# Kernel optimization log

Measured on AMD Instinct MI355X. Metric: run time of the kernel, lower is better.

Reference implementation:

```python
import jax, jax.numpy as jnp
import numpy as np

EPS = 1e-5  # BatchNorm2d default eps


def _median_pool3x3(x):
    # x: [B,1,H,W]; 3x3 kernel, stride 1, pad 1 (zero padding, matching F.unfold).
    B, C, H, W = x.shape
    xp = jnp.pad(x, ((0, 0), (0, 0), (1, 1), (1, 1)))
    # Stack the 9 shifted views -> [B,C,H,W,9]; torch.median returns the LOWER
    # median, i.e. sorted index (9-1)//2 = 4 for 9 elements.
    patches = jnp.stack([xp[:, :, i:i + H, j:j + W]
                         for i in range(3) for j in range(3)], axis=-1)
    return jnp.sort(patches, axis=-1)[..., 4]


def _batchnorm_train(x, w, b):
    # BatchNorm2d(1) in training mode: biased variance over (B,H,W) per channel.
    m = jnp.mean(x, axis=(0, 2, 3), keepdims=True)
    v = jnp.mean((x - m) ** 2, axis=(0, 2, 3), keepdims=True)
    return (x - m) * jax.lax.rsqrt(v + EPS) * w.reshape(1, -1, 1, 1) + b.reshape(1, -1, 1, 1)


def _shift_grid_sample(x, xshift, yshift):
    # Faithful to Shift.forward + F.grid_sample(mode='bilinear',
    # padding_mode='zeros', align_corners=False).
    B, C, Nv, Nh = x.shape
    yreg = (jnp.arange(Nv, dtype=x.dtype) - yshift) * 10.0  # [Nv]
    xreg = (jnp.arange(Nh, dtype=x.dtype) - xshift) * 10.0  # [Nh]
    Hv, Wv = Nv * 10.0, Nh * 10.0  # virtual upsampled size used for normalization
    gy = 2.0 * yreg / Hv - 1.0
    gx = 2.0 * xreg / Wv - 1.0
    # unnormalize (align_corners=False): pix = ((g+1)*size - 1)/2
    iy = ((gy + 1.0) * Nv - 1.0) * 0.5  # [Nv]
    ix = ((gx + 1.0) * Nh - 1.0) * 0.5  # [Nh]
    IY, IX = jnp.meshgrid(iy, ix, indexing='ij')  # [Nv,Nh] each

    x0 = jnp.floor(IX); x1 = x0 + 1.0
    y0 = jnp.floor(IY); y1 = y0 + 1.0
    wx1 = IX - x0; wx0 = 1.0 - wx1
    wy1 = IY - y0; wy0 = 1.0 - wy1

    def gather(yc, xc):
        valid = ((yc >= 0) & (yc < Nv) & (xc >= 0) & (xc < Nh)).astype(x.dtype)
        yi = jnp.clip(yc, 0, Nv - 1).astype(jnp.int32)
        xi = jnp.clip(xc, 0, Nh - 1).astype(jnp.int32)
        return x[:, :, yi, xi] * valid  # [B,C,Nv,Nh], zeros outside

    return (gather(y0, x0) * (wy0 * wx0) + gather(y0, x1) * (wy0 * wx1)
            + gather(y1, x0) * (wy1 * wx0) + gather(y1, x1) * (wy1 * wx1))


def setup_inputs() -> dict:
    key = jax.random.key(0)
    ks = jax.random.split(key, 4)
    B, Nv, Nh = 131072, 8, 16
    num_classes, channels = 8, Nv * Nh
    x = jax.random.normal(ks[0], (B, 1, Nv, Nh), dtype=jnp.float32)
    bn_weight = jnp.ones((1,), dtype=jnp.float32)
    bn_bias = jnp.zeros((1,), dtype=jnp.float32)
    xshift = jax.random.uniform(ks[1], (1,), dtype=jnp.float32)
    yshift = jax.random.uniform(ks[2], (1,), dtype=jnp.float32)
    fc_w = jax.random.normal(ks[3], (num_classes, channels), dtype=jnp.float32) / np.sqrt(channels)
    fc_b = jnp.zeros((num_classes,), dtype=jnp.float32)
    return {"x": x, "bn_weight": bn_weight, "bn_bias": bn_bias,
            "xshift": xshift, "yshift": yshift, "fc_w": fc_w, "fc_b": fc_b}


def reference(x, bn_weight, bn_bias, xshift, yshift, fc_w, fc_b):
    h = _median_pool3x3(x)
    h = _batchnorm_train(h, bn_weight, bn_bias)
    h = _shift_grid_sample(h, xshift, yshift)
    h = h.reshape(h.shape[0], -1)  # [B, Nv*Nh]
    return h @ fc_w.T + fc_b  # [B, num_classes]
```

## Files before the change

### kernel.cpp

```cpp
#include <hip/hip_runtime.h>
#include <math.h>

#define NIMG 131072
#define NBLK 512


__device__ __forceinline__ float med3f(float a, float b, float c) {
  return __builtin_amdgcn_fmed3f(a, b, c);
}
__device__ __forceinline__ float min3f(float a, float b, float c) { return fminf(fminf(a, b), c); }
__device__ __forceinline__ float max3f(float a, float b, float c) { return fmaxf(fmaxf(a, b), c); }

__device__ __forceinline__ void fold_weights(int p, const float* __restrict__ fc_w,
                                             float sx, float sy, float* __restrict__ w8) {
  const int y = p >> 4, x = p & 15;
  const int dY = (sy > 1.0f) ? 2 : 1;
  const int dX = (sx > 1.0f) ? 2 : 1;
  const float wy1 = (float)dY - sy, wy0 = 1.0f - wy1;
  const float wx1 = (float)dX - sx, wx0 = 1.0f - wx1;
  const int   iys[2] = { y + dY - 1, y + dY };
  const float wys[2] = { wy1, wy0 };
  const int   jxs[2] = { x + dX - 1, x + dX };
  const float wxs[2] = { wx1, wx0 };
  #pragma unroll
  for (int c = 0; c < 8; ++c) {
    float acc = 0.0f;
    #pragma unroll
    for (int a = 0; a < 2; ++a) {
      if (iys[a] < 0 || iys[a] >= 8) continue;
      #pragma unroll
      for (int b = 0; b < 2; ++b) {
        if (jxs[b] < 0 || jxs[b] >= 16) continue;
        acc += wys[a] * wxs[b] * fc_w[c * 128 + iys[a] * 16 + jxs[b]];
      }
    }
    w8[c] = acc;
  }
}

__global__ __launch_bounds__(256, 2) void k_main(const float* __restrict__ x,
                                                 const float* __restrict__ fcw,
                                                 const float* __restrict__ xs,
                                                 const float* __restrict__ ys,
                                                 float* __restrict__ out,
                                                 float* __restrict__ partial) {
  __shared__ float wlds[128 * 8];
  __shared__ float sred[8];
  const int tid = threadIdx.x;
  const int w = tid >> 6, l = tid & 63;
  const int img = blockIdx.x * 256 + tid;
  const float* __restrict__ xi = x + (size_t)img * 128;

  float rows[4][16];
  #pragma unroll
  for (int rr = 0; rr < 2; ++rr)
    #pragma unroll
    for (int q = 0; q < 4; ++q)
      *(float4*)&rows[rr][q * 4] = *(const float4*)&xi[rr * 16 + q * 4];

  if (tid < 128) {
    float w8[8];
    fold_weights(tid, fcw, xs[0] + 0.5f, ys[0] + 0.5f, w8);
    #pragma unroll
    for (int c = 0; c < 8; ++c) wlds[tid * 8 + c] = w8[c];
  }
  __syncthreads();

  float acc[8];
  #pragma unroll
  for (int c = 0; c < 8; ++c) acc[c] = 0.0f;
  float ssum = 0.0f, ssq = 0.0f;

  #pragma unroll
  for (int r = 0; r < 8; ++r) {
    if (r < 6) {
      #pragma unroll
      for (int q = 0; q < 4; ++q)
        *(float4*)&rows[(r + 2) & 3][q * 4] = *(const float4*)&xi[(r + 2) * 16 + q * 4];
    }
    float lo[16], mi[16], hi[16];
    #pragma unroll
    for (int c = 0; c < 16; ++c) {
      const float a = (r == 0) ? 0.0f : rows[(r - 1) & 3][c];
      const float b = rows[r & 3][c];
      const float d = (r == 7) ? 0.0f : rows[(r + 1) & 3][c];
      lo[c] = min3f(a, b, d);
      mi[c] = med3f(a, b, d);
      hi[c] = max3f(a, b, d);
    }
    #pragma unroll
    for (int j = 0; j < 16; ++j) {
      const float l0 = (j == 0) ? 0.0f : lo[j - 1];
      const float l2 = (j == 15) ? 0.0f : lo[j + 1];
      const float m0 = (j == 0) ? 0.0f : mi[j - 1];
      const float m2 = (j == 15) ? 0.0f : mi[j + 1];
      const float h0 = (j == 0) ? 0.0f : hi[j - 1];
      const float h2 = (j == 15) ? 0.0f : hi[j + 1];
      const float mx = max3f(l0, lo[j], l2);
      const float md = med3f(m0, mi[j], m2);
      const float mn = min3f(h0, hi[j], h2);
      const float med = med3f(mx, md, mn);
      ssum += med;
      ssq = fmaf(med, med, ssq);
      const float4 w0 = *(const float4*)&wlds[(r * 16 + j) * 8];
      const float4 w1 = *(const float4*)&wlds[(r * 16 + j) * 8 + 4];
      acc[0] = fmaf(med, w0.x, acc[0]);
      acc[1] = fmaf(med, w0.y, acc[1]);
      acc[2] = fmaf(med, w0.z, acc[2]);
      acc[3] = fmaf(med, w0.w, acc[3]);
      acc[4] = fmaf(med, w1.x, acc[4]);
      acc[5] = fmaf(med, w1.y, acc[5]);
      acc[6] = fmaf(med, w1.z, acc[6]);
      acc[7] = fmaf(med, w1.w, acc[7]);
    }
  }

  float4* o4 = (float4*)&out[(size_t)img * 8];
  o4[0] = make_float4(acc[0], acc[1], acc[2], acc[3]);
  o4[1] = make_float4(acc[4], acc[5], acc[6], acc[7]);

  #pragma unroll
  for (int off = 32; off; off >>= 1) {
    ssum += __shfl_xor(ssum, off, 64);
    ssq  += __shfl_xor(ssq,  off, 64);
  }
  if (l == 0) { sred[w] = ssum; sred[4 + w] = ssq; }
  __syncthreads();
  if (tid == 0) partial[2 * blockIdx.x]     = (sred[0] + sred[1]) + (sred[2] + sred[3]);
  if (tid == 1) partial[2 * blockIdx.x + 1] = (sred[4] + sred[5]) + (sred[6] + sred[7]);
}

__global__ __launch_bounds__(256) void k_scale(float* __restrict__ out,
                                               const float* __restrict__ partial,
                                               const float* __restrict__ fcw,
                                               const float* __restrict__ xs,
                                               const float* __restrict__ ys,
                                               const float* __restrict__ fcb,
                                               const float* __restrict__ bnw,
                                               const float* __restrict__ bnb) {
  __shared__ float sred[8];
  __shared__ float wred[4][8];
  __shared__ float fin[2];
  const int tid = threadIdx.x;
  const int w = tid >> 6, l = tid & 63;

  float s = partial[2 * tid]     + partial[2 * (tid + 256)];
  float q = partial[2 * tid + 1] + partial[2 * (tid + 256) + 1];
  #pragma unroll
  for (int off = 32; off; off >>= 1) {
    s += __shfl_xor(s, off, 64);
    q += __shfl_xor(q, off, 64);
  }

  float v[8];
  if (tid < 128) {
    fold_weights(tid, fcw, xs[0] + 0.5f, ys[0] + 0.5f, v);
  } else {
    #pragma unroll
    for (int c = 0; c < 8; ++c) v[c] = 0.0f;
  }
  #pragma unroll
  for (int c = 0; c < 8; ++c) {
    #pragma unroll
    for (int off = 32; off; off >>= 1) v[c] += __shfl_xor(v[c], off, 64);
  }

  if (l == 0) {
    sred[w] = s; sred[4 + w] = q;
    #pragma unroll
    for (int c = 0; c < 8; ++c) wred[w][c] = v[c];
  }
  __syncthreads();
  if (tid == 0) {
    const float S = (sred[0] + sred[1]) + (sred[2] + sred[3]);
    const float Q = (sred[4] + sred[5]) + (sred[6] + sred[7]);
    const float N = 16777216.0f;
    const float mm = S / N;
    const float vv = Q / N - mm * mm;
    const float a = bnw[0] / sqrtf(vv + 1e-5f);
    fin[0] = a;
    fin[1] = bnb[0] - mm * a;
  }
  __syncthreads();
  const float alpha = fin[0], beta = fin[1];

  const int i = blockIdx.x * 256 + tid;
  const int g = (i & 1) ? 4 : 0;
  float4 cv;
  cv.x = fmaf(beta, (wred[0][g + 0] + wred[1][g + 0]) + (wred[2][g + 0] + wred[3][g + 0]), fcb[g + 0]);
  cv.y = fmaf(beta, (wred[0][g + 1] + wred[1][g + 1]) + (wred[2][g + 1] + wred[3][g + 1]), fcb[g + 1]);
  cv.z = fmaf(beta, (wred[0][g + 2] + wred[1][g + 2]) + (wred[2][g + 2] + wred[3][g + 2]), fcb[g + 2]);
  cv.w = fmaf(beta, (wred[0][g + 3] + wred[1][g + 3]) + (wred[2][g + 3] + wred[3][g + 3]), fcb[g + 3]);

  float4* o4 = (float4*)out;
  float4 ov = o4[i];
  ov.x = fmaf(alpha, ov.x, cv.x);
  ov.y = fmaf(alpha, ov.y, cv.y);
  ov.z = fmaf(alpha, ov.z, cv.z);
  ov.w = fmaf(alpha, ov.w, cv.w);
  o4[i] = ov;
}

extern "C" void kernel_launch(void* const* d_in, const int* in_sizes, int n_in,
                              void* d_out, int out_size, void* d_ws, size_t ws_size,
                              hipStream_t stream) {
  const float* x   = (const float*)d_in[0];
  const float* bnw = (const float*)d_in[1];
  const float* bnb = (const float*)d_in[2];
  const float* xs  = (const float*)d_in[3];
  const float* ys  = (const float*)d_in[4];
  const float* fcw = (const float*)d_in[5];
  const float* fcb = (const float*)d_in[6];
  float* out = (float*)d_out;
  float* ws  = (float*)d_ws;

  float* partial = ws;

  hipLaunchKernelGGL(k_main,  dim3(NBLK), dim3(256), 0, stream, x, fcw, xs, ys, out, partial);
  hipLaunchKernelGGL(k_scale, dim3(1024), dim3(256), 0, stream, out, partial, fcw, xs, ys, fcb, bnw, bnb);
}
```

Before: 32.41 us.

## Drop block barriers via per-wave weight folding and per-wave partial sums

k_main now has every wave fold its own copy of the 128x8 combined weights into a private LDS slice, which removes both __syncthreads calls. Each wave also writes its own sum and sum-of-squares partial, and all 8 input rows are loaded up front into registers instead of a rolling 4-row buffer. k_scale reduces 2048 partials and processes 4 float4 outputs per thread with 256 blocks instead of 1024. The cost is redundant weight-folding work per wave, 16KB of LDS per block, and higher register pressure that could lower occupancy.

```diff
diff --git a/kernel.cpp b/kernel.cpp
--- a/kernel.cpp
+++ b/kernel.cpp
@@ -1,7 +1,6 @@
 #include <hip/hip_runtime.h>
 #include <math.h>
 
-#define NIMG 131072
 #define NBLK 512
 
 
@@ -44,27 +43,31 @@
                                                  const float* __restrict__ ys,
                                                  float* __restrict__ out,
                                                  float* __restrict__ partial) {
-  __shared__ float wlds[128 * 8];
-  __shared__ float sred[8];
+  __shared__ float wlds[4096];
   const int tid = threadIdx.x;
   const int w = tid >> 6, l = tid & 63;
   const int img = blockIdx.x * 256 + tid;
   const float* __restrict__ xi = x + (size_t)img * 128;
 
-  float rows[4][16];
-  #pragma unroll
-  for (int rr = 0; rr < 2; ++rr)
+  float rows[8][16];
+  #pragma unroll
+  for (int r = 0; r < 8; ++r)
     #pragma unroll
     for (int q = 0; q < 4; ++q)
-      *(float4*)&rows[rr][q * 4] = *(const float4*)&xi[rr * 16 + q * 4];
-
-  if (tid < 128) {
-    float w8[8];
-    fold_weights(tid, fcw, xs[0] + 0.5f, ys[0] + 0.5f, w8);
-    #pragma unroll
-    for (int c = 0; c < 8; ++c) wlds[tid * 8 + c] = w8[c];
-  }
-  __syncthreads();
+      *(float4*)&rows[r][q * 4] = *(const float4*)&xi[r * 16 + q * 4];
+
+  const float sx = xs[0] + 0.5f, sy = ys[0] + 0.5f;
+  {
+    float wa[8], wb[8];
+    fold_weights(2 * l,     fcw, sx, sy, wa);
+    fold_weights(2 * l + 1, fcw, sx, sy, wb);
+    float* base = &wlds[w * 1024 + l * 16];
+    *(float4*)&base[0]  = make_float4(wa[0], wa[1], wa[2], wa[3]);
+    *(float4*)&base[4]  = make_float4(wa[4], wa[5], wa[6], wa[7]);
+    *(float4*)&base[8]  = make_float4(wb[0], wb[1], wb[2], wb[3]);
+    *(float4*)&base[12] = make_float4(wb[4], wb[5], wb[6], wb[7]);
+  }
+  const float* __restrict__ wv = &wlds[w * 1024];
 
   float acc[8];
   #pragma unroll
@@ -73,17 +76,12 @@
 
   #pragma unroll
   for (int r = 0; r < 8; ++r) {
-    if (r < 6) {
-      #pragma unroll
-      for (int q = 0; q < 4; ++q)
-        *(float4*)&rows[(r + 2) & 3][q * 4] = *(const float4*)&xi[(r + 2) * 16 + q * 4];
-    }
     float lo[16], mi[16], hi[16];
     #pragma unroll
     for (int c = 0; c < 16; ++c) {
-      const float a = (r == 0) ? 0.0f : rows[(r - 1) & 3][c];
-      const float b = rows[r & 3][c];
-      const float d = (r == 7) ? 0.0f : rows[(r + 1) & 3][c];
+      const float a = (r == 0) ? 0.0f : rows[r - 1][c];
+      const float b = rows[r][c];
+      const float d = (r == 7) ? 0.0f : rows[r + 1][c];
       lo[c] = min3f(a, b, d);
       mi[c] = med3f(a, b, d);
       hi[c] = max3f(a, b, d);
@@ -102,8 +100,8 @@
       const float med = med3f(mx, md, mn);
       ssum += med;
       ssq = fmaf(med, med, ssq);
-      const float4 w0 = *(const float4*)&wlds[(r * 16 + j) * 8];
-      const float4 w1 = *(const float4*)&wlds[(r * 16 + j) * 8 + 4];
+      const float4 w0 = *(const float4*)&wv[(r * 16 + j) * 8];
+      const float4 w1 = *(const float4*)&wv[(r * 16 + j) * 8 + 4];
       acc[0] = fmaf(med, w0.x, acc[0]);
       acc[1] = fmaf(med, w0.y, acc[1]);
       acc[2] = fmaf(med, w0.z, acc[2]);
@@ -124,10 +122,11 @@
     ssum += __shfl_xor(ssum, off, 64);
     ssq  += __shfl_xor(ssq,  off, 64);
   }
-  if (l == 0) { sred[w] = ssum; sred[4 + w] = ssq; }
-  __syncthreads();
-  if (tid == 0) partial[2 * blockIdx.x]     = (sred[0] + sred[1]) + (sred[2] + sred[3]);
-  if (tid == 1) partial[2 * blockIdx.x + 1] = (sred[4] + sred[5]) + (sred[6] + sred[7]);
+  if (l == 0) {
+    const int wg = blockIdx.x * 4 + w;
+    partial[2 * wg]     = ssum;
+    partial[2 * wg + 1] = ssq;
+  }
 }
 
 __global__ __launch_bounds__(256) void k_scale(float* __restrict__ out,
@@ -144,8 +143,13 @@
   const int tid = threadIdx.x;
   const int w = tid >> 6, l = tid & 63;
 
-  float s = partial[2 * tid]     + partial[2 * (tid + 256)];
-  float q = partial[2 * tid + 1] + partial[2 * (tid + 256) + 1];
+  float s = 0.0f, q = 0.0f;
+  #pragma unroll
+  for (int k = 0; k < 8; ++k) {
+    const int idx = tid + 256 * k;
+    s += partial[2 * idx];
+    q += partial[2 * idx + 1];
+  }
   #pragma unroll
   for (int off = 32; off; off >>= 1) {
     s += __shfl_xor(s, off, 64);
@@ -184,21 +188,28 @@
   __syncthreads();
   const float alpha = fin[0], beta = fin[1];
 
-  const int i = blockIdx.x * 256 + tid;
-  const int g = (i & 1) ? 4 : 0;
-  float4 cv;
-  cv.x = fmaf(beta, (wred[0][g + 0] + wred[1][g + 0]) + (wred[2][g + 0] + wred[3][g + 0]), fcb[g + 0]);
-  cv.y = fmaf(beta, (wred[0][g + 1] + wred[1][g + 1]) + (wred[2][g + 1] + wred[3][g + 1]), fcb[g + 1]);
-  cv.z = fmaf(beta, (wred[0][g + 2] + wred[1][g + 2]) + (wred[2][g + 2] + wred[3][g + 2]), fcb[g + 2]);
-  cv.w = fmaf(beta, (wred[0][g + 3] + wred[1][g + 3]) + (wred[2][g + 3] + wred[3][g + 3]), fcb[g + 3]);
+  float cv[8];
+  #pragma unroll
+  for (int c = 0; c < 8; ++c) {
+    const float wsum = (wred[0][c] + wred[1][c]) + (wred[2][c] + wred[3][c]);
+    cv[c] = fmaf(beta, wsum, fcb[c]);
+  }
+  const float4 cv0 = make_float4(cv[0], cv[1], cv[2], cv[3]);
+  const float4 cv1 = make_float4(cv[4], cv[5], cv[6], cv[7]);
 
   float4* o4 = (float4*)out;
-  float4 ov = o4[i];
-  ov.x = fmaf(alpha, ov.x, cv.x);
-  ov.y = fmaf(alpha, ov.y, cv.y);
-  ov.z = fmaf(alpha, ov.z, cv.z);
-  ov.w = fmaf(alpha, ov.w, cv.w);
-  o4[i] = ov;
+  const int base = (blockIdx.x * 256 + tid) * 4;
+  #pragma unroll
+  for (int k = 0; k < 4; ++k) {
+    const int i = base + k;
+    const float4 c = (i & 1) ? cv1 : cv0;
+    float4 ov = o4[i];
+    ov.x = fmaf(alpha, ov.x, c.x);
+    ov.y = fmaf(alpha, ov.y, c.y);
+    ov.z = fmaf(alpha, ov.z, c.z);
+    ov.w = fmaf(alpha, ov.w, c.w);
+    o4[i] = ov;
+  }
 }
 
 extern "C" void kernel_launch(void* const* d_in, const int* in_sizes, int n_in,
@@ -217,5 +228,5 @@
   float* partial = ws;
 
   hipLaunchKernelGGL(k_main,  dim3(NBLK), dim3(256), 0, stream, x, fcw, xs, ys, out, partial);
-  hipLaunchKernelGGL(k_scale, dim3(1024), dim3(256), 0, stream, out, partial, fcw, xs, ys, fcb, bnw, bnb);
-}
+  hipLaunchKernelGGL(k_scale, dim3(256),  dim3(256), 0, stream, out, partial, fcw, xs, ys, fcb, bnw, bnb);
+}
```

After: 42.76 us. 31.9% more time.
